# Kernel optimization log

Hardware: AMD Instinct MI355X
Metric: run time of the kernel (lower is better)

Reference implementation:

```python
import jax, jax.numpy as jnp
import numpy as np

S, HID, H, KH, D = 2048, 3584, 28, 4, 128
G = H // KH  # GQA group size = 7
EPS = 1e-6
THETA = 1000000.0


def _rmsnorm(x, w, eps=EPS):
    v = jnp.mean(x.astype(jnp.float32) ** 2, axis=-1, keepdims=True)
    return (x * jax.lax.rsqrt(v + eps)).astype(x.dtype) * w


def setup_inputs() -> dict:
    key = jax.random.key(0)
    k1, k2, k3, k4 = jax.random.split(key, 4)
    return {
        "positions": jnp.arange(S, dtype=jnp.int32),
        "hidden_states": jax.random.normal(k1, (S, HID), dtype=jnp.float32),
        "qkv_w": jax.random.normal(k2, ((H + 2 * KH) * D, HID), dtype=jnp.float32) * (1.0 / np.sqrt(HID)),
        "qkv_b": jax.random.normal(k3, ((H + 2 * KH) * D,), dtype=jnp.float32) * 0.02,
        "q_norm_w": jnp.ones((H * D,), dtype=jnp.float32),
        "k_norm_w": jnp.ones((KH * D,), dtype=jnp.float32),
        "o_w": jax.random.normal(k4, (HID, H * D), dtype=jnp.float32) * (1.0 / np.sqrt(H * D)),
    }


def reference(positions, hidden_states, qkv_w, qkv_b, q_norm_w, k_norm_w, o_w):
    # QKV projection (fused linear, bias=True)
    qkv = hidden_states @ qkv_w.T + qkv_b  # [S, (H+2*KH)*D]
    q, k, v = jnp.split(qkv, [H * D, H * D + KH * D], axis=-1)

    # olmo-style QK RMSNorm over the full (all-heads-concatenated) q/k vectors
    q = _rmsnorm(q, q_norm_w)
    k = _rmsnorm(k, k_norm_w)

    # NeoX-style RoPE (vLLM default): rotate halves
    half = D // 2
    inv_freq = 1.0 / (THETA ** (jnp.arange(0, D, 2, dtype=jnp.float32) / D))  # [D/2]
    freqs = positions[:, None].astype(jnp.float32) * inv_freq  # [S, D/2]
    cos = jnp.cos(freqs)[:, None, :]  # [S, 1, D/2]
    sin = jnp.sin(freqs)[:, None, :]

    def rope(x, nh):
        x = x.reshape(S, nh, D)
        x1, x2 = x[..., :half], x[..., half:]
        return jnp.concatenate([x1 * cos - x2 * sin, x2 * cos + x1 * sin], axis=-1)

    q = rope(q, H)            # [S, H, D]
    k = rope(k, KH)           # [S, KH, D]
    v = v.reshape(S, KH, D)   # [S, KH, D]

    # Grouped-query causal attention
    qg = q.reshape(S, KH, G, D)
    scores = jnp.einsum('skgd,tkd->kgst', qg, k) * (D ** -0.5)  # [KH, G, S, S]
    causal = positions[:, None] >= positions[None, :]  # [S, S]
    scores = jnp.where(causal[None, None], scores, jnp.finfo(scores.dtype).min)
    probs = jax.nn.softmax(scores, axis=-1)
    attn = jnp.einsum('kgst,tkd->skgd', probs, v).reshape(S, H * D)

    # Output projection (bias=False)
    return attn @ o_w.T  # [S, HID]
```

## Files before the change

kernel.cpp:

```cpp
#include <hip/hip_runtime.h>
#include <hip/hip_bf16.h>
#include <stdint.h>

#define S_LEN 2048
#define HIDDEN 3584
#define NH 28
#define NKH 4
#define DH 128
#define NG 7
#define NQKV 4608
#define QD 3584
#define KD 512

using bf16x8 = __attribute__((ext_vector_type(8))) __bf16;
using f32x4  = __attribute__((ext_vector_type(4))) float;
using f32x16 = __attribute__((ext_vector_type(16))) float;

#define AS3(p) ((__attribute__((address_space(3))) void*)(p))
#define AS1(p) ((const __attribute__((address_space(1))) void*)(p))

__device__ __forceinline__ unsigned short f2bf(float f) {
    unsigned u = __float_as_uint(f);
    u += 0x7FFFu + ((u >> 16) & 1u);
    return (unsigned short)(u >> 16);
}
__device__ __forceinline__ unsigned cvtpk(float a, float b) {
    unsigned r;
    asm("v_cvt_pk_bf16_f32 %0, %1, %2" : "=v"(r) : "v"(a), "v"(b));
    return r;
}

__global__ void cvt2_f32_bf16(const float* __restrict__ a, unsigned short* __restrict__ oa, int na4,
                              const float* __restrict__ b, unsigned short* __restrict__ ob, int nb4) {
    int i = blockIdx.x * blockDim.x + threadIdx.x;
    const float* src;
    unsigned short* dst;
    int n;
    if (i < na4)            { src = a; dst = oa; n = i; }
    else if (i < na4 + nb4) { src = b; dst = ob; n = i - na4; }
    else return;
    float4 v = ((const float4*)src)[n];
    ushort4 o;
    o.x = f2bf(v.x); o.y = f2bf(v.y); o.z = f2bf(v.z); o.w = f2bf(v.w);
    ((ushort4*)dst)[n] = o;
}

__global__ void cvt_f32_bf16(const float* __restrict__ in,
                             unsigned short* __restrict__ out, int n4) {
    int i = blockIdx.x * blockDim.x + threadIdx.x;
    if (i >= n4) return;
    float4 v = ((const float4*)in)[i];
    ushort4 o;
    o.x = f2bf(v.x); o.y = f2bf(v.y); o.z = f2bf(v.z); o.w = f2bf(v.w);
    ((ushort4*)out)[i] = o;
}

template<int BN>
__global__ __launch_bounds__(512, 2) void gemm_big(
    const unsigned short* __restrict__ A,
    const unsigned short* __restrict__ B,
    float* __restrict__ C,
    const float* __restrict__ bias,
    int M, int N, int K)
{
    constexpr int NF    = BN / 64;
    constexpr int WN    = BN / 4;
    constexpr int BBLK  = BN / 8;
    constexpr int SBLK  = 32 + BBLK;
    constexpr int SPW   = SBLK / 8;
    constexpr int TILEB = SBLK * 1024;

    __shared__ __align__(16) unsigned char dsmem[2 * TILEB];

    const int tid  = threadIdx.x;
    const int w    = tid >> 6;
    const int lane = tid & 63;
    const int lr   = lane & 15;
    const int lg   = lane >> 4;
    const int wr   = w >> 2;
    const int wc   = w & 3;
    const int m0   = blockIdx.y * 256;
    const int n0   = blockIdx.x * BN;
    const long K2  = (long)K * 2;

    const int srow = lane >> 3;
    const int scw  = 16 * ((lane & 7) ^ srow);
    const unsigned char* Ab = (const unsigned char*)A;
    const unsigned char* Bb = (const unsigned char*)B;

    auto stage = [&](int kt, unsigned char* buf) {
        const long kb = (long)kt * 128;
        #pragma unroll
        for (int j = 0; j < SPW; ++j) {
            const int blk = w * SPW + j;
            const unsigned char* src = (blk < 32)
                ? Ab + (long)(m0 + blk * 8 + srow) * K2 + kb + scw
                : Bb + (long)(n0 + (blk - 32) * 8 + srow) * K2 + kb + scw;
            __builtin_amdgcn_global_load_lds(AS1(src), AS3(buf + blk * 1024), 16, 0, 0);
        }
    };

    f32x4 acc[8][NF] = {};

    stage(0, dsmem);
    stage(1, dsmem + TILEB);
    if constexpr (SPW == 7) asm volatile("s_waitcnt vmcnt(7)" ::: "memory");
    else                    asm volatile("s_waitcnt vmcnt(6)" ::: "memory");
    __builtin_amdgcn_s_barrier();

    const int nk = K >> 6;
    for (int kt = 0; kt < nk; ++kt) {
        unsigned char* buf = dsmem + (kt & 1) * TILEB;
        const unsigned char* As = buf;
        const unsigned char* Bs = buf + 32768;

        bf16x8 a[8][2], bfr[NF][2];
        #pragma unroll
        for (int mi = 0; mi < 8; ++mi) {
            const int row = wr * 128 + mi * 16 + lr;
            #pragma unroll
            for (int kk = 0; kk < 2; ++kk)
                a[mi][kk] = *(const bf16x8*)(As + row * 128 +
                                             ((kk * 64 + lg * 16) ^ ((lr & 7) << 4)));
        }
        #pragma unroll
        for (int ni = 0; ni < NF; ++ni) {
            const int row = wc * WN + ni * 16 + lr;
            #pragma unroll
            for (int kk = 0; kk < 2; ++kk)
                bfr[ni][kk] = *(const bf16x8*)(Bs + row * 128 +
                                               ((kk * 64 + lg * 16) ^ ((lr & 7) << 4)));
        }

        __builtin_amdgcn_s_setprio(1);
        #pragma unroll
        for (int mi = 0; mi < 4; ++mi)
            #pragma unroll
            for (int ni = 0; ni < NF; ++ni)
                #pragma unroll
                for (int kk = 0; kk < 2; ++kk)
                    acc[mi][ni] = __builtin_amdgcn_mfma_f32_16x16x32_bf16(
                        a[mi][kk], bfr[ni][kk], acc[mi][ni], 0, 0, 0);
        __builtin_amdgcn_s_setprio(0);

        asm volatile("s_waitcnt lgkmcnt(0)" ::: "memory");
        __builtin_amdgcn_s_barrier();

        if (kt + 2 < nk) stage(kt + 2, buf);

        __builtin_amdgcn_s_setprio(1);
        #pragma unroll
        for (int mi = 4; mi < 8; ++mi)
            #pragma unroll
            for (int ni = 0; ni < NF; ++ni)
                #pragma unroll
                for (int kk = 0; kk < 2; ++kk)
                    acc[mi][ni] = __builtin_amdgcn_mfma_f32_16x16x32_bf16(
                        a[mi][kk], bfr[ni][kk], acc[mi][ni], 0, 0, 0);
        __builtin_amdgcn_s_setprio(0);

        if (kt + 2 < nk) {
            if constexpr (SPW == 7) asm volatile("s_waitcnt vmcnt(7)" ::: "memory");
            else                    asm volatile("s_waitcnt vmcnt(6)" ::: "memory");
        } else {
            asm volatile("s_waitcnt vmcnt(0)" ::: "memory");
        }
        __builtin_amdgcn_s_barrier();
    }

    #pragma unroll
    for (int mi = 0; mi < 8; ++mi) {
        #pragma unroll
        for (int ni = 0; ni < NF; ++ni) {
            const int col = n0 + wc * WN + ni * 16 + lr;
            const float bv = bias ? bias[col] : 0.0f;
            #pragma unroll
            for (int j = 0; j < 4; ++j) {
                const int row = m0 + wr * 128 + mi * 16 + lg * 4 + j;
                C[(long)row * N + col] = acc[mi][ni][j] + bv;
            }
        }
    }
}

__global__ __launch_bounds__(256) void qkv_post(
    const float* __restrict__ qkv,
    const int* __restrict__ positions,
    const float* __restrict__ qnw,
    const float* __restrict__ knw,
    unsigned short* __restrict__ qb,
    unsigned short* __restrict__ kb,
    unsigned short* __restrict__ vt2)
{
    const int s   = blockIdx.x;
    const int tid = threadIdx.x;
    const float* rowp = qkv + (long)s * NQKV;
    __shared__ float red[256];
    __shared__ float s_rq, s_rk;

    float aq = 0.f;
    for (int i = tid; i < QD; i += 256) { float v = rowp[i]; aq += v * v; }
    red[tid] = aq; __syncthreads();
    for (int off = 128; off > 0; off >>= 1) {
        if (tid < off) red[tid] += red[tid + off];
        __syncthreads();
    }
    if (tid == 0) s_rq = rsqrtf(red[0] / (float)QD + 1e-6f);
    __syncthreads();

    float ak = 0.f;
    for (int i = tid; i < KD; i += 256) { float v = rowp[QD + i]; ak += v * v; }
    red[tid] = ak; __syncthreads();
    for (int off = 128; off > 0; off >>= 1) {
        if (tid < off) red[tid] += red[tid + off];
        __syncthreads();
    }
    if (tid == 0) s_rk = rsqrtf(red[0] / (float)KD + 1e-6f);
    __syncthreads();

    const float rq  = s_rq, rk = s_rk * 0.08838834764831845f;
    const float pos = (float)positions[s];
    const float c_lnf = 0.21586735253866598f;

    for (int u = tid; u < NH * 64; u += 256) {
        const int h = u >> 6, j = u & 63;
        const float inv = expf(-(float)j * c_lnf);
        float sn, cs;
        sincosf(pos * inv, &sn, &cs);
        const float x1 = rowp[h * DH + j]      * rq * qnw[h * DH + j];
        const float x2 = rowp[h * DH + 64 + j] * rq * qnw[h * DH + 64 + j];
        qb[((long)h * S_LEN + s) * DH + j]      = f2bf(x1 * cs - x2 * sn);
        qb[((long)h * S_LEN + s) * DH + 64 + j] = f2bf(x2 * cs + x1 * sn);
    }
    for (int u = tid; u < NKH * 64; u += 256) {
        const int h = u >> 6, j = u & 63;
        const float inv = expf(-(float)j * c_lnf);
        float sn, cs;
        sincosf(pos * inv, &sn, &cs);
        const float x1 = rowp[QD + h * DH + j]      * rk * knw[h * DH + j];
        const float x2 = rowp[QD + h * DH + 64 + j] * rk * knw[h * DH + 64 + j];
        kb[((long)h * S_LEN + s) * DH + j]      = f2bf(x1 * cs - x2 * sn);
        kb[((long)h * S_LEN + s) * DH + 64 + j] = f2bf(x2 * cs + x1 * sn);
    }
    for (int u = tid; u < KD; u += 256) {
        const int hh = u >> 7, d = u & 127;
        vt2[(((long)hh * (S_LEN / 32) + (s >> 5)) * DH + d) * 32 + (s & 31)] =
            f2bf(rowp[QD + KD + u]);
    }
}

__global__ __launch_bounds__(512) void attn_fwd(
    const unsigned short* __restrict__ qb,
    const unsigned short* __restrict__ kb,
    const unsigned short* __restrict__ vt2,
    unsigned short* __restrict__ attnb)
{
    __shared__ __align__(16) unsigned char sK[2][8192];
    __shared__ __align__(16) unsigned char sV[2][8192];

    const int qt   = 63 - blockIdx.x;
    const int kh   = blockIdx.y;
    const int tid  = threadIdx.x;
    const int w    = tid >> 6;
    const int lane = tid & 63;
    const int lq   = lane & 31;
    const int hi   = lane >> 5;
    const int hi8  = hi * 8;
    const int hi4  = hi * 4;
    const int q0   = qt * 32;
    const int NT   = qt + 1;

    const unsigned char* kgb = (const unsigned char*)(kb + (long)kh * S_LEN * DH);
    const unsigned char* vgb = (const unsigned char*)vt2 + (long)kh * (S_LEN / 32) * 8192;

    const int ksrc_off = (((tid & 15) ^ (tid >> 4)) & 15) << 4;
    const int u        = tid & 255;
    const int vsrc_off = ((u & 3) ^ ((u >> 3) & 3)) << 4;

    const float RTHR = 8.0f;

    bf16x8 qf[8];
    if (w < 7) {
        const int h = kh * NG + w;
        const unsigned short* qrow = qb + ((long)h * S_LEN + q0 + lq) * DH;
        #pragma unroll
        for (int c = 0; c < 8; ++c)
            qf[c] = *(const bf16x8*)(qrow + c * 16 + hi8);
    }

    f32x16 o[4] = {};
    float m = -3e38f;
    float l = 0.f;

    if (tid < 256) {
        #pragma unroll
        for (int j = 0; j < 2; ++j)
            __builtin_amdgcn_global_load_lds(AS1(kgb + ((tid >> 4) + 16 * j) * 256 + ksrc_off),
                                             AS3(&sK[0][0] + w * 1024 + j * 4096), 16, 0, 0);
    } else {
        #pragma unroll
        for (int j = 0; j < 2; ++j)
            __builtin_amdgcn_global_load_lds(AS1(vgb + ((u >> 2) + 64 * j) * 64 + vsrc_off),
                                             AS3(&sV[0][0] + (w - 4) * 1024 + j * 4096), 16, 0, 0);
    }

    for (int t = 0; t < NT; ++t) {
        __syncthreads();

        if (t + 1 < NT) {
            const int b = (t + 1) & 1;
            if (tid < 256) {
                const unsigned char* ks = kgb + (long)(t + 1) * 8192;
                #pragma unroll
                for (int j = 0; j < 2; ++j)
                    __builtin_amdgcn_global_load_lds(AS1(ks + ((tid >> 4) + 16 * j) * 256 + ksrc_off),
                                                     AS3(&sK[b][0] + w * 1024 + j * 4096), 16, 0, 0);
            } else {
                const unsigned char* vs = vgb + (long)(t + 1) * 8192;
                #pragma unroll
                for (int j = 0; j < 2; ++j)
                    __builtin_amdgcn_global_load_lds(AS1(vs + ((u >> 2) + 64 * j) * 64 + vsrc_off),
                                                     AS3(&sV[b][0] + (w - 4) * 1024 + j * 4096), 16, 0, 0);
            }
        }

        if (w < 7) {
            const unsigned char* sKb = sK[t & 1];
            const unsigned char* sVb = sV[t & 1];

            bf16x8 kf[8];
            #pragma unroll
            for (int c = 0; c < 8; ++c)
                kf[c] = *(const bf16x8*)(sKb + lq * 256 + (((2 * c + hi) ^ (lq & 15)) << 4));
            f32x16 sc = {};
            #pragma unroll
            for (int c = 0; c < 8; ++c)
                sc = __builtin_amdgcn_mfma_f32_32x32x16_bf16(kf[c], qf[c], sc, 0, 0, 0);

            float s[16];
            if (t == NT - 1) {
                #pragma unroll
                for (int r = 0; r < 16; ++r) {
                    const int kr = (r & 3) + 8 * (r >> 2) + hi4;
                    s[r] = (kr > lq) ? -3e38f : sc[r];
                }
            } else {
                #pragma unroll
                for (int r = 0; r < 16; ++r) s[r] = sc[r];
            }

            float mx = s[0];
            #pragma unroll
            for (int r = 1; r < 16; ++r) mx = fmaxf(mx, s[r]);
            mx = fmaxf(mx, __shfl_xor(mx, 32));

            if (!__all(mx <= m + RTHR)) {
                const float nm  = fmaxf(m, mx);
                const float fac = __expf(m - nm);
                l *= fac;
                #pragma unroll
                for (int d0 = 0; d0 < 4; ++d0)
                    #pragma unroll
                    for (int r = 0; r < 16; ++r) o[d0][r] *= fac;
                m = nm;
            }

            float p[16];
            float ps = 0.f;
            #pragma unroll
            for (int r = 0; r < 16; ++r) {
                p[r] = __expf(s[r] - m);
                ps += p[r];
            }
            ps += __shfl_xor(ps, 32);
            l += ps;

            unsigned pa01 = cvtpk(p[0],  p[1]),  pa23 = cvtpk(p[2],  p[3]);
            unsigned pb01 = cvtpk(p[4],  p[5]),  pb23 = cvtpk(p[6],  p[7]);
            unsigned pc01 = cvtpk(p[8],  p[9]),  pc23 = cvtpk(p[10], p[11]);
            unsigned pd01 = cvtpk(p[12], p[13]), pd23 = cvtpk(p[14], p[15]);
            unsigned xa01 = __shfl_xor((int)pa01, 32), xa23 = __shfl_xor((int)pa23, 32);
            unsigned xb01 = __shfl_xor((int)pb01, 32), xb23 = __shfl_xor((int)pb23, 32);
            unsigned xc01 = __shfl_xor((int)pc01, 32), xc23 = __shfl_xor((int)pc23, 32);
            unsigned xd01 = __shfl_xor((int)pd01, 32), xd23 = __shfl_xor((int)pd23, 32);

            union { unsigned uu[4]; bf16x8 v; } pf0, pf1;
            pf0.uu[0] = hi ? xb01 : pa01;
            pf0.uu[1] = hi ? xb23 : pa23;
            pf0.uu[2] = hi ? pb01 : xa01;
            pf0.uu[3] = hi ? pb23 : xa23;
            pf1.uu[0] = hi ? xd01 : pc01;
            pf1.uu[1] = hi ? xd23 : pc23;
            pf1.uu[2] = hi ? pd01 : xc01;
            pf1.uu[3] = hi ? pd23 : xc23;

            #pragma unroll
            for (int d0 = 0; d0 < 4; ++d0) {
                const int row = d0 * 32 + lq;
                const int sw  = (lq >> 1) & 3;
                bf16x8 vf0 = *(const bf16x8*)(sVb + row * 64 + ((hi ^ sw) << 4));
                bf16x8 vf1 = *(const bf16x8*)(sVb + row * 64 + (((2 + hi) ^ sw) << 4));
                o[d0] = __builtin_amdgcn_mfma_f32_32x32x16_bf16(vf0, pf0.v, o[d0], 0, 0, 0);
                o[d0] = __builtin_amdgcn_mfma_f32_32x32x16_bf16(vf1, pf1.v, o[d0], 0, 0, 0);
            }
        }
    }

    if (w == 7) return;

    const float rl = 1.0f / l;
    unsigned short* orow = attnb + (long)(q0 + lq) * QD + (kh * NG + w) * DH;
    #pragma unroll
    for (int d0 = 0; d0 < 4; ++d0) {
        #pragma unroll
        for (int g = 0; g < 4; ++g) {
            ushort4 s4;
            s4.x = f2bf(o[d0][4 * g + 0] * rl);
            s4.y = f2bf(o[d0][4 * g + 1] * rl);
            s4.z = f2bf(o[d0][4 * g + 2] * rl);
            s4.w = f2bf(o[d0][4 * g + 3] * rl);
            *(ushort4*)(orow + d0 * 32 + 8 * g + hi4) = s4;
        }
    }
}

extern "C" void kernel_launch(void* const* d_in, const int* in_sizes, int n_in,
                              void* d_out, int out_size, void* d_ws, size_t ws_size,
                              hipStream_t stream) {
    const int*   positions = (const int*)d_in[0];
    const float* hidden    = (const float*)d_in[1];
    const float* qkv_w     = (const float*)d_in[2];
    const float* qkv_b     = (const float*)d_in[3];
    const float* qnw       = (const float*)d_in[4];
    const float* knw       = (const float*)d_in[5];
    const float* o_w       = (const float*)d_in[6];
    float* out = (float*)d_out;

    unsigned char* ws = (unsigned char*)d_ws;
    unsigned short* hb    = (unsigned short*)(ws);
    unsigned short* w1    = (unsigned short*)(ws + 14680064);
    float*          qkvf  = (float*)(ws + 47710208);
    unsigned short* qbuf  = (unsigned short*)(ws + 85458944);
    unsigned short* kbuf  = (unsigned short*)(ws + 100139008);
    unsigned short* vtb   = (unsigned short*)(ws + 102236160);
    unsigned short* attnb = (unsigned short*)(ws);
    unsigned short* w2    = (unsigned short*)(ws + 14680064);

    const int na4 = S_LEN * HIDDEN / 4;
    const int nb4 = NQKV * HIDDEN / 4;
    cvt2_f32_bf16<<<(na4 + nb4 + 255) / 256, 256, 0, stream>>>(hidden, hb, na4, qkv_w, w1, nb4);
    gemm_big<192><<<dim3(NQKV / 192, S_LEN / 256), 512, 0, stream>>>(
        hb, w1, qkvf, qkv_b, S_LEN, NQKV, HIDDEN);
    qkv_post<<<S_LEN, 256, 0, stream>>>(qkvf, positions, qnw, knw, qbuf, kbuf, vtb);
    attn_fwd<<<dim3(S_LEN / 32, NKH), 512, 0, stream>>>(qbuf, kbuf, vtb, attnb);
    cvt_f32_bf16<<<(HIDDEN * QD / 4 + 255) / 256, 256, 0, stream>>>(o_w, w2, HIDDEN * QD / 4);
    gemm_big<128><<<dim3(HIDDEN / 128, S_LEN / 256), 512, 0, stream>>>(
        attnb, w2, out, nullptr, S_LEN, HIDDEN, QD);
}
```

Baseline: 281.7 us.

## Switch GEMMs to 256x256 tiles with quarter-staged ping-pong pipeline

Replaces the templated GEMM with a fixed 256x256 tile kernel that splits each k-tile's LDS staging into four quarter loads interleaved with four MFMA quadrants. This lets the loads for the next tile overlap compute at finer granularity, and each loaded tile is reused across more output. The cost is many more barriers per iteration, 128KB of LDS per block, and fewer blocks: 18x8 and 14x8, so the grid may not fill all CUs. The pair loop assumes an even number of k-tiles, which holds for both K values here.

```diff
diff --git a/kernel.cpp b/kernel.cpp
--- a/kernel.cpp
+++ b/kernel.cpp
@@ -55,22 +55,14 @@
     ((ushort4*)out)[i] = o;
 }
 
-template<int BN>
-__global__ __launch_bounds__(512, 2) void gemm_big(
+__global__ __launch_bounds__(512, 2) void gemm256(
     const unsigned short* __restrict__ A,
     const unsigned short* __restrict__ B,
     float* __restrict__ C,
     const float* __restrict__ bias,
     int M, int N, int K)
 {
-    constexpr int NF    = BN / 64;
-    constexpr int WN    = BN / 4;
-    constexpr int BBLK  = BN / 8;
-    constexpr int SBLK  = 32 + BBLK;
-    constexpr int SPW   = SBLK / 8;
-    constexpr int TILEB = SBLK * 1024;
-
-    __shared__ __align__(16) unsigned char dsmem[2 * TILEB];
+    __shared__ __align__(16) unsigned char dsmem[131072];
 
     const int tid  = threadIdx.x;
     const int w    = tid >> 6;
@@ -80,99 +72,140 @@
     const int wr   = w >> 2;
     const int wc   = w & 3;
     const int m0   = blockIdx.y * 256;
-    const int n0   = blockIdx.x * BN;
+    const int n0   = blockIdx.x * 256;
     const long K2  = (long)K * 2;
-
     const int srow = lane >> 3;
     const int scw  = 16 * ((lane & 7) ^ srow);
     const unsigned char* Ab = (const unsigned char*)A;
     const unsigned char* Bb = (const unsigned char*)B;
-
-    auto stage = [&](int kt, unsigned char* buf) {
+    const int nk = K >> 6;
+
+    const unsigned char* buf0 = dsmem;
+    const unsigned char* buf1 = dsmem + 65536;
+
+    auto stage_half = [&](int kt, int h, int bi) {
         const long kb = (long)kt * 128;
-        #pragma unroll
-        for (int j = 0; j < SPW; ++j) {
-            const int blk = w * SPW + j;
-            const unsigned char* src = (blk < 32)
-                ? Ab + (long)(m0 + blk * 8 + srow) * K2 + kb + scw
-                : Bb + (long)(n0 + (blk - 32) * 8 + srow) * K2 + kb + scw;
-            __builtin_amdgcn_global_load_lds(AS1(src), AS3(buf + blk * 1024), 16, 0, 0);
+        unsigned char* dst = dsmem + bi * 65536 + h * 16384;
+        #pragma unroll
+        for (int j = 0; j < 2; ++j) {
+            const int blk = w * 2 + j;
+            const unsigned char* src = (h < 2)
+                ? Ab + (long)(m0 + h * 128 + blk * 8 + srow) * K2 + kb + scw
+                : Bb + (long)(n0 + (h - 2) * 128 + blk * 8 + srow) * K2 + kb + scw;
+            __builtin_amdgcn_global_load_lds(AS1(src), AS3(dst + blk * 1024), 16, 0, 0);
         }
     };
 
-    f32x4 acc[8][NF] = {};
-
-    stage(0, dsmem);
-    stage(1, dsmem + TILEB);
-    if constexpr (SPW == 7) asm volatile("s_waitcnt vmcnt(7)" ::: "memory");
-    else                    asm volatile("s_waitcnt vmcnt(6)" ::: "memory");
+    f32x4  acc[8][4] = {};
+    bf16x8 afr[4][2];
+    bf16x8 bA[2][2];
+    bf16x8 bB[2][2];
+
+    auto read_a = [&](const unsigned char* bufp, int mih) {
+        #pragma unroll
+        for (int i = 0; i < 4; ++i) {
+            const int row = wr * 128 + (mih * 4 + i) * 16 + lr;
+            #pragma unroll
+            for (int kk = 0; kk < 2; ++kk)
+                afr[i][kk] = *(const bf16x8*)(bufp + row * 128 +
+                                              ((kk * 64 + lg * 16) ^ ((lr & 7) << 4)));
+        }
+    };
+    auto read_b = [&](const unsigned char* bufp, int nih, bf16x8 (&dstf)[2][2]) {
+        #pragma unroll
+        for (int i = 0; i < 2; ++i) {
+            const int row = wc * 64 + (nih * 2 + i) * 16 + lr;
+            #pragma unroll
+            for (int kk = 0; kk < 2; ++kk)
+                dstf[i][kk] = *(const bf16x8*)(bufp + 32768 + row * 128 +
+                                               ((kk * 64 + lg * 16) ^ ((lr & 7) << 4)));
+        }
+    };
+    auto quad = [&](bf16x8 (&bq)[2][2], int mib, int nib) {
+        __builtin_amdgcn_s_setprio(1);
+        #pragma unroll
+        for (int i = 0; i < 4; ++i)
+            #pragma unroll
+            for (int n2 = 0; n2 < 2; ++n2)
+                #pragma unroll
+                for (int kk = 0; kk < 2; ++kk)
+                    acc[mib + i][nib + n2] = __builtin_amdgcn_mfma_f32_16x16x32_bf16(
+                        afr[i][kk], bq[n2][kk], acc[mib + i][nib + n2], 0, 0, 0);
+        __builtin_amdgcn_s_setprio(0);
+    };
+
+    #pragma unroll
+    for (int h = 0; h < 4; ++h) stage_half(0, h, 0);
+    stage_half(1, 0, 1);
+    asm volatile("s_waitcnt vmcnt(2)" ::: "memory");
     __builtin_amdgcn_s_barrier();
 
-    const int nk = K >> 6;
-    for (int kt = 0; kt < nk; ++kt) {
-        unsigned char* buf = dsmem + (kt & 1) * TILEB;
-        const unsigned char* As = buf;
-        const unsigned char* Bs = buf + 32768;
-
-        bf16x8 a[8][2], bfr[NF][2];
-        #pragma unroll
-        for (int mi = 0; mi < 8; ++mi) {
-            const int row = wr * 128 + mi * 16 + lr;
-            #pragma unroll
-            for (int kk = 0; kk < 2; ++kk)
-                a[mi][kk] = *(const bf16x8*)(As + row * 128 +
-                                             ((kk * 64 + lg * 16) ^ ((lr & 7) << 4)));
-        }
-        #pragma unroll
-        for (int ni = 0; ni < NF; ++ni) {
-            const int row = wc * WN + ni * 16 + lr;
-            #pragma unroll
-            for (int kk = 0; kk < 2; ++kk)
-                bfr[ni][kk] = *(const bf16x8*)(Bs + row * 128 +
-                                               ((kk * 64 + lg * 16) ^ ((lr & 7) << 4)));
-        }
-
-        __builtin_amdgcn_s_setprio(1);
-        #pragma unroll
-        for (int mi = 0; mi < 4; ++mi)
-            #pragma unroll
-            for (int ni = 0; ni < NF; ++ni)
-                #pragma unroll
-                for (int kk = 0; kk < 2; ++kk)
-                    acc[mi][ni] = __builtin_amdgcn_mfma_f32_16x16x32_bf16(
-                        a[mi][kk], bfr[ni][kk], acc[mi][ni], 0, 0, 0);
-        __builtin_amdgcn_s_setprio(0);
-
-        asm volatile("s_waitcnt lgkmcnt(0)" ::: "memory");
-        __builtin_amdgcn_s_barrier();
-
-        if (kt + 2 < nk) stage(kt + 2, buf);
-
-        __builtin_amdgcn_s_setprio(1);
-        #pragma unroll
-        for (int mi = 4; mi < 8; ++mi)
-            #pragma unroll
-            for (int ni = 0; ni < NF; ++ni)
-                #pragma unroll
-                for (int kk = 0; kk < 2; ++kk)
-                    acc[mi][ni] = __builtin_amdgcn_mfma_f32_16x16x32_bf16(
-                        a[mi][kk], bfr[ni][kk], acc[mi][ni], 0, 0, 0);
-        __builtin_amdgcn_s_setprio(0);
-
-        if (kt + 2 < nk) {
-            if constexpr (SPW == 7) asm volatile("s_waitcnt vmcnt(7)" ::: "memory");
-            else                    asm volatile("s_waitcnt vmcnt(6)" ::: "memory");
-        } else {
-            asm volatile("s_waitcnt vmcnt(0)" ::: "memory");
-        }
+    const int npairs = nk >> 1;
+    for (int p = 0; p < npairs; ++p) {
+        const int t1 = 2 * p + 1;
+        int t2 = 2 * p + 2; if (t2 >= nk) t2 = nk - 1;
+        int t3 = 2 * p + 3; if (t3 >= nk) t3 = nk - 1;
+
+        read_a(buf0, 0); read_b(buf0, 0, bA);
+        stage_half(t1, 1, 1);
+        __builtin_amdgcn_s_barrier();
+        asm volatile("s_waitcnt lgkmcnt(0)" ::: "memory");
+        __builtin_amdgcn_sched_barrier(0);
+        quad(bA, 0, 0);
+        __builtin_amdgcn_s_barrier();
+        read_b(buf0, 1, bB);
+        stage_half(t1, 2, 1);
+        __builtin_amdgcn_s_barrier();
+        asm volatile("s_waitcnt lgkmcnt(0)" ::: "memory");
+        __builtin_amdgcn_sched_barrier(0);
+        quad(bB, 0, 2);
+        __builtin_amdgcn_s_barrier();
+        read_a(buf0, 1);
+        stage_half(t1, 3, 1);
+        __builtin_amdgcn_s_barrier();
+        asm volatile("s_waitcnt lgkmcnt(0)" ::: "memory");
+        __builtin_amdgcn_sched_barrier(0);
+        quad(bA, 4, 0);
+        __builtin_amdgcn_s_barrier();
+        stage_half(t2, 0, 0);
+        __builtin_amdgcn_s_barrier();
+        quad(bB, 4, 2);
+        asm volatile("s_waitcnt vmcnt(2)" ::: "memory");
+        __builtin_amdgcn_s_barrier();
+
+        read_a(buf1, 0); read_b(buf1, 0, bA);
+        stage_half(t2, 1, 0);
+        __builtin_amdgcn_s_barrier();
+        asm volatile("s_waitcnt lgkmcnt(0)" ::: "memory");
+        __builtin_amdgcn_sched_barrier(0);
+        quad(bA, 0, 0);
+        __builtin_amdgcn_s_barrier();
+        read_b(buf1, 1, bB);
+        stage_half(t2, 2, 0);
+        __builtin_amdgcn_s_barrier();
+        asm volatile("s_waitcnt lgkmcnt(0)" ::: "memory");
+        __builtin_amdgcn_sched_barrier(0);
+        quad(bB, 0, 2);
+        __builtin_amdgcn_s_barrier();
+        read_a(buf1, 1);
+        stage_half(t2, 3, 0);
+        __builtin_amdgcn_s_barrier();
+        asm volatile("s_waitcnt lgkmcnt(0)" ::: "memory");
+        __builtin_amdgcn_sched_barrier(0);
+        quad(bA, 4, 0);
+        __builtin_amdgcn_s_barrier();
+        stage_half(t3, 0, 1);
+        __builtin_amdgcn_s_barrier();
+        quad(bB, 4, 2);
+        asm volatile("s_waitcnt vmcnt(2)" ::: "memory");
         __builtin_amdgcn_s_barrier();
     }
 
     #pragma unroll
     for (int mi = 0; mi < 8; ++mi) {
         #pragma unroll
-        for (int ni = 0; ni < NF; ++ni) {
-            const int col = n0 + wc * WN + ni * 16 + lr;
+        for (int ni = 0; ni < 4; ++ni) {
+            const int col = n0 + wc * 64 + ni * 16 + lr;
             const float bv = bias ? bias[col] : 0.0f;
             #pragma unroll
             for (int j = 0; j < 4; ++j) {
@@ -449,11 +482,11 @@
     const int na4 = S_LEN * HIDDEN / 4;
     const int nb4 = NQKV * HIDDEN / 4;
     cvt2_f32_bf16<<<(na4 + nb4 + 255) / 256, 256, 0, stream>>>(hidden, hb, na4, qkv_w, w1, nb4);
-    gemm_big<192><<<dim3(NQKV / 192, S_LEN / 256), 512, 0, stream>>>(
+    gemm256<<<dim3(NQKV / 256, S_LEN / 256), 512, 0, stream>>>(
         hb, w1, qkvf, qkv_b, S_LEN, NQKV, HIDDEN);
     qkv_post<<<S_LEN, 256, 0, stream>>>(qkvf, positions, qnw, knw, qbuf, kbuf, vtb);
     attn_fwd<<<dim3(S_LEN / 32, NKH), 512, 0, stream>>>(qbuf, kbuf, vtb, attnb);
     cvt_f32_bf16<<<(HIDDEN * QD / 4 + 255) / 256, 256, 0, stream>>>(o_w, w2, HIDDEN * QD / 4);
-    gemm_big<128><<<dim3(HIDDEN / 128, S_LEN / 256), 512, 0, stream>>>(
+    gemm256<<<dim3(HIDDEN / 256, S_LEN / 256), 512, 0, stream>>>(
         attnb, w2, out, nullptr, S_LEN, HIDDEN, QD);
 }
```

Result: slower. 315.5 us (+12.0%).

## Restructure bf16 GEMM main loop into split A/B staging with half-tile interleaving

Applied to the files above, without the earlier changes.

Replaces the GEMM K-loop with a two-tile-per-iteration schedule. A and B are staged separately into LDS, and each tile's MFMA work is split into two halves. Global-to-LDS loads for the next tiles are issued between the half-tile LDS reads and MFMA bursts, so memory traffic overlaps compute more finely and fewer fragment registers are held live at once. The cost is more barriers per iteration and tighter vmcnt bookkeeping. The pair loop also assumes an even tile count, and the clamping of out-of-range tile indices causes redundant loads at the tail.

```diff
diff --git a/kernel.cpp b/kernel.cpp
--- a/kernel.cpp
+++ b/kernel.cpp
@@ -56,7 +56,7 @@
 }
 
 template<int BN>
-__global__ __launch_bounds__(512, 2) void gemm_big(
+__global__ __launch_bounds__(512, 2) void gemm_deep(
     const unsigned short* __restrict__ A,
     const unsigned short* __restrict__ B,
     float* __restrict__ C,
@@ -65,12 +65,9 @@
 {
     constexpr int NF    = BN / 64;
     constexpr int WN    = BN / 4;
-    constexpr int BBLK  = BN / 8;
-    constexpr int SBLK  = 32 + BBLK;
-    constexpr int SPW   = SBLK / 8;
-    constexpr int TILEB = SBLK * 1024;
-
-    __shared__ __align__(16) unsigned char dsmem[2 * TILEB];
+    constexpr int VB    = BN / 64;
+    constexpr int TILEB = (256 + BN) * 128;
+    __shared__ __align__(16) unsigned char ds[2 * TILEB];
 
     const int tid  = threadIdx.x;
     const int w    = tid >> 6;
@@ -82,91 +79,111 @@
     const int m0   = blockIdx.y * 256;
     const int n0   = blockIdx.x * BN;
     const long K2  = (long)K * 2;
-
-    const int srow = lane >> 3;
-    const int scw  = 16 * ((lane & 7) ^ srow);
+    const int scw  = 16 * ((tid & 7) ^ ((tid >> 3) & 7));
+    const int srow = tid >> 3;
     const unsigned char* Ab = (const unsigned char*)A;
     const unsigned char* Bb = (const unsigned char*)B;
-
-    auto stage = [&](int kt, unsigned char* buf) {
+    const int nk = K >> 6;
+
+    unsigned char* buf0 = ds;
+    unsigned char* buf1 = ds + TILEB;
+
+    auto stageB = [&](int kt, unsigned char* bufp) {
         const long kb = (long)kt * 128;
         #pragma unroll
-        for (int j = 0; j < SPW; ++j) {
-            const int blk = w * SPW + j;
-            const unsigned char* src = (blk < 32)
-                ? Ab + (long)(m0 + blk * 8 + srow) * K2 + kb + scw
-                : Bb + (long)(n0 + (blk - 32) * 8 + srow) * K2 + kb + scw;
-            __builtin_amdgcn_global_load_lds(AS1(src), AS3(buf + blk * 1024), 16, 0, 0);
-        }
+        for (int k = 0; k < VB; ++k)
+            __builtin_amdgcn_global_load_lds(
+                AS1(Bb + (long)(n0 + k * 64 + srow) * K2 + kb + scw),
+                AS3(bufp + k * 8192 + w * 1024), 16, 0, 0);
     };
-
-    f32x4 acc[8][NF] = {};
-
-    stage(0, dsmem);
-    stage(1, dsmem + TILEB);
-    if constexpr (SPW == 7) asm volatile("s_waitcnt vmcnt(7)" ::: "memory");
-    else                    asm volatile("s_waitcnt vmcnt(6)" ::: "memory");
-    __builtin_amdgcn_s_barrier();
-
-    const int nk = K >> 6;
-    for (int kt = 0; kt < nk; ++kt) {
-        unsigned char* buf = dsmem + (kt & 1) * TILEB;
-        const unsigned char* As = buf;
-        const unsigned char* Bs = buf + 32768;
-
-        bf16x8 a[8][2], bfr[NF][2];
-        #pragma unroll
-        for (int mi = 0; mi < 8; ++mi) {
-            const int row = wr * 128 + mi * 16 + lr;
+    auto stageA = [&](int kt, unsigned char* bufp) {
+        const long kb = (long)kt * 128;
+        #pragma unroll
+        for (int k = 0; k < 4; ++k)
+            __builtin_amdgcn_global_load_lds(
+                AS1(Ab + (long)(m0 + k * 64 + srow) * K2 + kb + scw),
+                AS3(bufp + VB * 8192 + k * 8192 + w * 1024), 16, 0, 0);
+    };
+
+    f32x4  acc[8][NF] = {};
+    bf16x8 af[4][2], bf[NF][2];
+
+    auto readA = [&](const unsigned char* bufp, int half) {
+        #pragma unroll
+        for (int i = 0; i < 4; ++i) {
+            const int row = wr * 128 + (half * 4 + i) * 16 + lr;
             #pragma unroll
             for (int kk = 0; kk < 2; ++kk)
-                a[mi][kk] = *(const bf16x8*)(As + row * 128 +
+                af[i][kk] = *(const bf16x8*)(bufp + VB * 8192 + row * 128 +
                                              ((kk * 64 + lg * 16) ^ ((lr & 7) << 4)));
         }
+    };
+    auto readB = [&](const unsigned char* bufp) {
         #pragma unroll
         for (int ni = 0; ni < NF; ++ni) {
             const int row = wc * WN + ni * 16 + lr;
             #pragma unroll
             for (int kk = 0; kk < 2; ++kk)
-                bfr[ni][kk] = *(const bf16x8*)(Bs + row * 128 +
-                                               ((kk * 64 + lg * 16) ^ ((lr & 7) << 4)));
-        }
-
+                bf[ni][kk] = *(const bf16x8*)(bufp + row * 128 +
+                                              ((kk * 64 + lg * 16) ^ ((lr & 7) << 4)));
+        }
+    };
+    auto mfmah = [&](int half) {
         __builtin_amdgcn_s_setprio(1);
         #pragma unroll
-        for (int mi = 0; mi < 4; ++mi)
+        for (int i = 0; i < 4; ++i)
             #pragma unroll
             for (int ni = 0; ni < NF; ++ni)
                 #pragma unroll
                 for (int kk = 0; kk < 2; ++kk)
-                    acc[mi][ni] = __builtin_amdgcn_mfma_f32_16x16x32_bf16(
-                        a[mi][kk], bfr[ni][kk], acc[mi][ni], 0, 0, 0);
+                    acc[half * 4 + i][ni] = __builtin_amdgcn_mfma_f32_16x16x32_bf16(
+                        af[i][kk], bf[ni][kk], acc[half * 4 + i][ni], 0, 0, 0);
         __builtin_amdgcn_s_setprio(0);
-
-        asm volatile("s_waitcnt lgkmcnt(0)" ::: "memory");
-        __builtin_amdgcn_s_barrier();
-
-        if (kt + 2 < nk) stage(kt + 2, buf);
-
-        __builtin_amdgcn_s_setprio(1);
-        #pragma unroll
-        for (int mi = 4; mi < 8; ++mi)
-            #pragma unroll
-            for (int ni = 0; ni < NF; ++ni)
-                #pragma unroll
-                for (int kk = 0; kk < 2; ++kk)
-                    acc[mi][ni] = __builtin_amdgcn_mfma_f32_16x16x32_bf16(
-                        a[mi][kk], bfr[ni][kk], acc[mi][ni], 0, 0, 0);
-        __builtin_amdgcn_s_setprio(0);
-
-        if (kt + 2 < nk) {
-            if constexpr (SPW == 7) asm volatile("s_waitcnt vmcnt(7)" ::: "memory");
-            else                    asm volatile("s_waitcnt vmcnt(6)" ::: "memory");
-        } else {
-            asm volatile("s_waitcnt vmcnt(0)" ::: "memory");
-        }
-        __builtin_amdgcn_s_barrier();
-    }
+    };
+
+    #define VMC() do { if constexpr (VB == 3) asm volatile("s_waitcnt vmcnt(3)" ::: "memory"); \
+                       else                   asm volatile("s_waitcnt vmcnt(2)" ::: "memory"); } while (0)
+    #define LGK0() do { asm volatile("s_waitcnt lgkmcnt(0)" ::: "memory"); \
+                        __builtin_amdgcn_sched_barrier(0); } while (0)
+
+    stageB(0, buf0); stageA(0, buf0); stageB(1, buf1);
+    VMC();
+    __builtin_amdgcn_s_barrier();
+
+    const int npairs = nk >> 1;
+    for (int p = 0; p < npairs; ++p) {
+        const int to = 2 * p + 1;
+        int te2 = 2 * p + 2; if (te2 >= nk) te2 = nk - 1;
+        int to2 = 2 * p + 3; if (to2 >= nk) to2 = nk - 1;
+
+        readA(buf0, 0); readB(buf0);
+        stageA(to, buf1);
+        __builtin_amdgcn_s_barrier();
+        LGK0();
+        mfmah(0);
+        __builtin_amdgcn_s_barrier();
+        readA(buf0, 1);
+        stageB(te2, buf0);
+        __builtin_amdgcn_s_barrier();
+        LGK0();
+        mfmah(1);
+        VMC();
+        __builtin_amdgcn_s_barrier();
+        readA(buf1, 0); readB(buf1);
+        stageA(te2, buf0);
+        __builtin_amdgcn_s_barrier();
+        LGK0();
+        mfmah(0);
+        __builtin_amdgcn_s_barrier();
+        readA(buf1, 1);
+        stageB(to2, buf1);
+        __builtin_amdgcn_s_barrier();
+        LGK0();
+        mfmah(1);
+        VMC();
+        __builtin_amdgcn_s_barrier();
+    }
+    asm volatile("s_waitcnt vmcnt(0)" ::: "memory");
 
     #pragma unroll
     for (int mi = 0; mi < 8; ++mi) {
@@ -181,6 +198,8 @@
             }
         }
     }
+    #undef VMC
+    #undef LGK0
 }
 
 __global__ __launch_bounds__(256) void qkv_post(
@@ -449,11 +468,11 @@
     const int na4 = S_LEN * HIDDEN / 4;
     const int nb4 = NQKV * HIDDEN / 4;
     cvt2_f32_bf16<<<(na4 + nb4 + 255) / 256, 256, 0, stream>>>(hidden, hb, na4, qkv_w, w1, nb4);
-    gemm_big<192><<<dim3(NQKV / 192, S_LEN / 256), 512, 0, stream>>>(
+    gemm_deep<192><<<dim3(NQKV / 192, S_LEN / 256), 512, 0, stream>>>(
         hb, w1, qkvf, qkv_b, S_LEN, NQKV, HIDDEN);
     qkv_post<<<S_LEN, 256, 0, stream>>>(qkvf, positions, qnw, knw, qbuf, kbuf, vtb);
     attn_fwd<<<dim3(S_LEN / 32, NKH), 512, 0, stream>>>(qbuf, kbuf, vtb, attnb);
     cvt_f32_bf16<<<(HIDDEN * QD / 4 + 255) / 256, 256, 0, stream>>>(o_w, w2, HIDDEN * QD / 4);
-    gemm_big<128><<<dim3(HIDDEN / 128, S_LEN / 256), 512, 0, stream>>>(
+    gemm_deep<128><<<dim3(HIDDEN / 128, S_LEN / 256), 512, 0, stream>>>(
         attnb, w2, out, nullptr, S_LEN, HIDDEN, QD);
 }
```

New measurement: 261.7 us. 7.1% less time.
